# Kernel tuning notes

Measured on AMD Instinct MI355X. Metric: run time of the kernel, lower is better.

The kernel has to match this reference:

```python
import jax, jax.numpy as jnp
import numpy as np

PAD = 0
VALUE_WEIGHT = 5.0
L, D, H, DF, V, T_MAX = 8, 1024, 16, 4096, 4096, 2048
HD = D // H


def _ln(x, w, b, eps=1e-5):
    mu = x.mean(-1, keepdims=True)
    var = ((x - mu) ** 2).mean(-1, keepdims=True)
    return (x - mu) * jax.lax.rsqrt(var + eps) * w + b


def setup_inputs() -> dict:
    key = jax.random.key(0)
    ks = jax.random.split(key, 16)
    s = 0.02
    inp = {
        'input_ids': jax.random.randint(ks[0], (4, 2048), 0, V),
        'targets': jax.random.randint(ks[1], (4, 2048), 0, V),
        'value_mask': jax.random.randint(ks[2], (4, 2048), 0, 2).astype(bool),
        'token_emb': jax.random.normal(ks[3], (V, D), jnp.float32) * s,
        'pos_emb': jax.random.normal(ks[4], (T_MAX, D), jnp.float32) * s,
        'ln1_w': jnp.ones((L, D), jnp.float32), 'ln1_b': jnp.zeros((L, D), jnp.float32),
        'wqkv': jax.random.normal(ks[5], (L, D, 3 * D), jnp.float32) * s,
        'bqkv': jnp.zeros((L, 3 * D), jnp.float32),
        'wproj': jax.random.normal(ks[6], (L, D, D), jnp.float32) * s,
        'bproj': jnp.zeros((L, D), jnp.float32),
        'ln2_w': jnp.ones((L, D), jnp.float32), 'ln2_b': jnp.zeros((L, D), jnp.float32),
        'w1': jax.random.normal(ks[7], (L, D, DF), jnp.float32) * s,
        'b1': jnp.zeros((L, DF), jnp.float32),
        'w2': jax.random.normal(ks[8], (L, DF, D), jnp.float32) * s,
        'b2': jnp.zeros((L, D), jnp.float32),
        'lnf_w': jnp.ones((D,), jnp.float32), 'lnf_b': jnp.zeros((D,), jnp.float32),
    }
    return inp


def reference(input_ids, targets, value_mask, token_emb, pos_emb, ln1_w, ln1_b,
              wqkv, bqkv, wproj, bproj, ln2_w, ln2_b, w1, b1, w2, b2, lnf_w, lnf_b):
    B, T = input_ids.shape
    x = token_emb[input_ids] + pos_emb[:T]  # (B,T,D)
    causal = jnp.triu(jnp.ones((T, T), bool), 1)  # True above diagonal -> masked
    scale = 1.0 / np.sqrt(HD)
    for l in range(L):
        h = _ln(x, ln1_w[l], ln1_b[l])
        qkv = h @ wqkv[l] + bqkv[l]  # (B,T,3D)
        q, k, v = jnp.split(qkv, 3, axis=-1)
        q = q.reshape(B, T, H, HD).transpose(0, 2, 1, 3)  # (B,H,T,HD)
        k = k.reshape(B, T, H, HD).transpose(0, 2, 1, 3)
        v = v.reshape(B, T, H, HD).transpose(0, 2, 1, 3)
        scores = jnp.einsum('bhqd,bhkd->bhqk', q, k) * scale
        scores = jnp.where(causal, -jnp.inf, scores)
        attn = jax.nn.softmax(scores, axis=-1)
        out = jnp.einsum('bhqk,bhkd->bhqd', attn, v)
        out = out.transpose(0, 2, 1, 3).reshape(B, T, D)
        x = x + out @ wproj[l] + bproj[l]
        h2 = _ln(x, ln2_w[l], ln2_b[l])
        x = x + jax.nn.gelu(h2 @ w1[l] + b1[l], approximate=False) @ w2[l] + b2[l]
    x = _ln(x, lnf_w, lnf_b)
    logits = x @ token_emb.T  # tied lm_head, (B,T,V)
    # weighted CE (ignore_index=PAD zeroes the per-token loss; weights sum over all tokens)
    logp = jax.nn.log_softmax(logits, axis=-1)
    nll = -jnp.take_along_axis(logp, targets[..., None], axis=-1)[..., 0]  # (B,T)
    ce = jnp.where(targets == PAD, 0.0, nll)
    weights = 1.0 + (VALUE_WEIGHT - 1.0) * value_mask.astype(jnp.float32)
    loss = (ce * weights).sum() / weights.sum()
    return logits, loss
```

## Files before the change

kernel.cpp:

```cpp
#include <hip/hip_runtime.h>
#include <hip/hip_bf16.h>

typedef unsigned short u16;
typedef short bf16x8 __attribute__((ext_vector_type(8)));
typedef float f32x4 __attribute__((ext_vector_type(4)));

__device__ inline float bflo(unsigned int w) { union { float f; unsigned int i; } c; c.i = w << 16; return c.f; }
__device__ inline float bfhi(unsigned int w) { union { float f; unsigned int i; } c; c.i = w & 0xffff0000u; return c.f; }
__device__ inline u16 f2bf(float f) {
    union { float f; unsigned int i; } c; c.f = f;
    unsigned int r = c.i + 0x7FFFu + ((c.i >> 16) & 1u);
    return (u16)(r >> 16);
}

__device__ inline float wave_sum(float v) {
#pragma unroll
    for (int off = 32; off; off >>= 1) v += __shfl_down(v, off);
    return v;
}

__device__ inline void gload16(const void* g, void* l) {
    __builtin_amdgcn_global_load_lds((const __attribute__((address_space(1))) void*)g,
                                     (__attribute__((address_space(3))) void*)l, 16, 0, 0);
}

__global__ __launch_bounds__(256) void k_cvt(const float* __restrict__ in, u16* __restrict__ out) {
    int i = blockIdx.x * 256 + threadIdx.x;
    float4 v = ((const float4*)in)[i];
    ushort4 o;
    o.x = f2bf(v.x); o.y = f2bf(v.y); o.z = f2bf(v.z); o.w = f2bf(v.w);
    ((ushort4*)out)[i] = o;
}

__global__ __launch_bounds__(256) void k_transpose(const float* __restrict__ in, u16* __restrict__ out, int R, int C) {
    __shared__ float tile[32][33];
    const float* inL = in + (size_t)blockIdx.z * R * C;
    u16* outL = out + (size_t)blockIdx.z * R * C;
    int cb = blockIdx.x * 32, rb = blockIdx.y * 32;
    int tx = threadIdx.x, ty = threadIdx.y;
#pragma unroll
    for (int i = 0; i < 32; i += 8)
        tile[ty + i][tx] = inL[(size_t)(rb + ty + i) * C + cb + tx];
    __syncthreads();
#pragma unroll
    for (int i = 0; i < 32; i += 8)
        outL[(size_t)(cb + ty + i) * R + rb + tx] = f2bf(tile[tx][ty + i]);
}

__global__ __launch_bounds__(256) void k_embed(const int* __restrict__ ids, const float* __restrict__ emb,
                                               const float* __restrict__ pos, float* __restrict__ x) {
    int i = blockIdx.x * 256 + threadIdx.x;
    int m = i >> 8;
    int d4 = i & 255;
    int t = m & 2047;
    int id = ids[m];
    float4 e = ((const float4*)(emb + (size_t)id * 1024))[d4];
    float4 p = ((const float4*)(pos + (size_t)t * 1024))[d4];
    float4 r; r.x = e.x + p.x; r.y = e.y + p.y; r.z = e.z + p.z; r.w = e.w + p.w;
    ((float4*)(x + (size_t)m * 1024))[d4] = r;
}

__global__ __launch_bounds__(256) void k_ln(const float* __restrict__ in, const float* __restrict__ w,
                                            const float* __restrict__ b, u16* __restrict__ out) {
    int row = blockIdx.x, tid = threadIdx.x;
    float4 v = ((const float4*)(in + (size_t)row * 1024))[tid];
    float s = v.x + v.y + v.z + v.w;
    float ss = v.x * v.x + v.y * v.y + v.z * v.z + v.w * v.w;
    s = wave_sum(s); ss = wave_sum(ss);
    __shared__ float rs[4], rss[4];
    int wid = tid >> 6, lane = tid & 63;
    if (lane == 0) { rs[wid] = s; rss[wid] = ss; }
    __syncthreads();
    s = rs[0] + rs[1] + rs[2] + rs[3];
    ss = rss[0] + rss[1] + rss[2] + rss[3];
    float mu = s * (1.0f / 1024.0f);
    float var = ss * (1.0f / 1024.0f) - mu * mu;
    float inv = rsqrtf(var + 1e-5f);
    float4 wv = ((const float4*)w)[tid], bv = ((const float4*)b)[tid];
    ushort4 o;
    o.x = f2bf((v.x - mu) * inv * wv.x + bv.x);
    o.y = f2bf((v.y - mu) * inv * wv.y + bv.y);
    o.z = f2bf((v.z - mu) * inv * wv.z + bv.z);
    o.w = f2bf((v.w - mu) * inv * wv.w + bv.w);
    *(ushort4*)(out + (size_t)row * 1024 + tid * 4) = o;
}

template <bool OUT_BF16, bool GELU, bool RES, bool BIAS>
__global__ __launch_bounds__(256, 2) void k_gemm(const u16* __restrict__ A, const u16* __restrict__ Bt,
                                                 const float* __restrict__ bias, const float* __restrict__ res,
                                                 float* __restrict__ outF, u16* __restrict__ outB,
                                                 int M, int N, int K) {
    __shared__ __align__(16) u16 ldsA[2][128 * 32];
    __shared__ __align__(16) u16 ldsB[2][128 * 32];
    int tid = threadIdx.x;
    int wave = tid >> 6, lane = tid & 63;
    int quad = lane >> 4, l15 = lane & 15;
    int m0 = blockIdx.y * 128, n0 = blockIdx.x * 128;
    int wm = (wave >> 1) * 64, wn = (wave & 1) * 64;

    f32x4 acc[4][4];
#pragma unroll
    for (int i = 0; i < 4; i++)
#pragma unroll
        for (int j = 0; j < 4; j++) acc[i][j] = (f32x4){0.f, 0.f, 0.f, 0.f};

    int r0 = tid >> 2, c0 = (tid & 3) * 8;
    const size_t half = (size_t)64 * K;
    const u16* pa0 = A + (size_t)(m0 + r0) * K + c0;
    const u16* pb0 = Bt + (size_t)(n0 + r0) * K + c0;
    const int woff = (tid & 0xC0) * 8;

#define STAGE(bi, k0)                              \
    {                                              \
        u16* la_ = ldsA[bi] + woff;                \
        u16* lb_ = ldsB[bi] + woff;                \
        gload16(pa0 + (k0), la_);                  \
        gload16(pa0 + half + (k0), la_ + 2048);    \
        gload16(pb0 + (k0), lb_);                  \
        gload16(pb0 + half + (k0), lb_ + 2048);    \
    }

    STAGE(0, 0);
    __syncthreads();

    const int nt = K >> 5;
    int cur = 0;
    for (int t = 0; t < nt; t++) {
        if (t + 1 < nt) STAGE(cur ^ 1, (t + 1) * 32);
        const u16* ca = ldsA[cur];
        const u16* cb = ldsB[cur];
        bf16x8 af[4], bfr[4];
#pragma unroll
        for (int i = 0; i < 4; i++) af[i] = *(const bf16x8*)(ca + (wm + i * 16 + l15) * 32 + quad * 8);
#pragma unroll
        for (int j = 0; j < 4; j++) bfr[j] = *(const bf16x8*)(cb + (wn + j * 16 + l15) * 32 + quad * 8);
#pragma unroll
        for (int i = 0; i < 4; i++)
#pragma unroll
            for (int j = 0; j < 4; j++)
                acc[i][j] = __builtin_amdgcn_mfma_f32_16x16x32_bf16(af[i], bfr[j], acc[i][j], 0, 0, 0);
        __syncthreads();
        cur ^= 1;
    }
#undef STAGE

#pragma unroll
    for (int j = 0; j < 4; j++) {
        int col = n0 + wn + j * 16 + l15;
        float bj = BIAS ? bias[col] : 0.f;
#pragma unroll
        for (int i = 0; i < 4; i++) {
#pragma unroll
            for (int r = 0; r < 4; r++) {
                int row = m0 + wm + i * 16 + quad * 4 + r;
                float v = acc[i][j][r] + bj;
                if (GELU) v = 0.5f * v * (1.0f + erff(v * 0.70710678f));
                if (RES) v += res[(size_t)row * N + col];
                if (OUT_BF16) outB[(size_t)row * N + col] = f2bf(v);
                else outF[(size_t)row * N + col] = v;
            }
        }
    }
}

__global__ __launch_bounds__(256, 2) void k_attn(const u16* __restrict__ qkv, u16* __restrict__ out) {
    const int b = blockIdx.y >> 4, h = blockIdx.y & 15;
    const int qt = gridDim.x - 1 - blockIdx.x;
    const int q0 = qt * 128;
    const int tid = threadIdx.x;
    const int wave = tid >> 6, lane = tid & 63;
    const int quad = lane >> 4, l15 = lane & 15;
    const int wrow = q0 + wave * 32;

    __shared__ __align__(16) u16 Klds[64 * 72];
    __shared__ __align__(16) u16 Vt[64 * 72];
    __shared__ __align__(16) u16 Plds[4][32 * 72];

    const u16* base = qkv + (size_t)b * 2048 * 3072 + h * 64;

    bf16x8 qf[2][2];
#pragma unroll
    for (int i = 0; i < 2; i++)
#pragma unroll
        for (int kc = 0; kc < 2; kc++)
            qf[i][kc] = *(const bf16x8*)(base + (size_t)(wrow + i * 16 + l15) * 3072 + kc * 32 + quad * 8);

    f32x4 o[2][4];
#pragma unroll
    for (int i = 0; i < 2; i++)
#pragma unroll
        for (int jd = 0; jd < 4; jd++) o[i][jd] = (f32x4){0.f, 0.f, 0.f, 0.f};
    float mrow[2][4], lrow[2][4];
#pragma unroll
    for (int i = 0; i < 2; i++)
#pragma unroll
        for (int r = 0; r < 4; r++) { mrow[i][r] = -3e38f; lrow[i][r] = 0.f; }

    const int kk_ = tid >> 2, kc0 = (tid & 3) * 16;
    const int vk = tid & 63, vc = (tid >> 6) * 16;

    const int ktiles = 2 * (qt + 1);
    for (int t = 0; t < ktiles; t++) {
        const int kt = t * 64;
        __syncthreads();
        {
            const u16* kp = base + 1024 + (size_t)(kt + kk_) * 3072 + kc0;
            uint4 a = *(const uint4*)kp;
            uint4 c = *(const uint4*)(kp + 8);
            *(uint4*)(Klds + kk_ * 72 + kc0) = a;
            *(uint4*)(Klds + kk_ * 72 + kc0 + 8) = c;
            const u16* vp = base + 2048 + (size_t)(kt + vk) * 3072 + vc;
            uint4 v0 = *(const uint4*)vp;
            uint4 v1 = *(const uint4*)(vp + 8);
            u16 tmp[16];
            *(uint4*)tmp = v0; *(uint4*)(tmp + 8) = v1;
#pragma unroll
            for (int e = 0; e < 16; e++) Vt[(vc + e) * 72 + vk] = tmp[e];
        }
        __syncthreads();

        if (kt <= wrow + 31) {
            f32x4 s[2][4];
#pragma unroll
            for (int i = 0; i < 2; i++)
#pragma unroll
                for (int j = 0; j < 4; j++) s[i][j] = (f32x4){0.f, 0.f, 0.f, 0.f};
#pragma unroll
            for (int kc = 0; kc < 2; kc++) {
                bf16x8 bf[4];
#pragma unroll
                for (int j = 0; j < 4; j++)
                    bf[j] = *(const bf16x8*)(Klds + (j * 16 + l15) * 72 + kc * 32 + quad * 8);
#pragma unroll
                for (int i = 0; i < 2; i++)
#pragma unroll
                    for (int j = 0; j < 4; j++)
                        s[i][j] = __builtin_amdgcn_mfma_f32_16x16x32_bf16(qf[i][kc], bf[j], s[i][j], 0, 0, 0);
            }
            const bool partial = (kt + 63 > wrow);
#pragma unroll
            for (int i = 0; i < 2; i++)
#pragma unroll
                for (int j = 0; j < 4; j++)
#pragma unroll
                    for (int r = 0; r < 4; r++) {
                        float v = s[i][j][r] * 0.125f;
                        if (partial) {
                            int row = wrow + i * 16 + quad * 4 + r;
                            int col = kt + j * 16 + l15;
                            if (col > row) v = -3e30f;
                        }
                        s[i][j][r] = v;
                    }
            u16* pw = Plds[wave];
#pragma unroll
            for (int i = 0; i < 2; i++)
#pragma unroll
                for (int r = 0; r < 4; r++) {
                    float mx = fmaxf(fmaxf(s[i][0][r], s[i][1][r]), fmaxf(s[i][2][r], s[i][3][r]));
                    mx = fmaxf(mx, __shfl_xor(mx, 1));
                    mx = fmaxf(mx, __shfl_xor(mx, 2));
                    mx = fmaxf(mx, __shfl_xor(mx, 4));
                    mx = fmaxf(mx, __shfl_xor(mx, 8));
                    float mnew = fmaxf(mrow[i][r], mx);
                    float alpha = __expf(mrow[i][r] - mnew);
                    mrow[i][r] = mnew;
                    float psum = 0.f;
#pragma unroll
                    for (int j = 0; j < 4; j++) {
                        float p = __expf(s[i][j][r] - mnew);
                        s[i][j][r] = p;
                        psum += p;
                    }
                    psum += __shfl_xor(psum, 1);
                    psum += __shfl_xor(psum, 2);
                    psum += __shfl_xor(psum, 4);
                    psum += __shfl_xor(psum, 8);
                    lrow[i][r] = lrow[i][r] * alpha + psum;
#pragma unroll
                    for (int jd = 0; jd < 4; jd++) o[i][jd][r] *= alpha;
                }
#pragma unroll
            for (int i = 0; i < 2; i++)
#pragma unroll
                for (int j = 0; j < 4; j++)
#pragma unroll
                    for (int r = 0; r < 4; r++)
                        pw[(i * 16 + quad * 4 + r) * 72 + j * 16 + l15] = f2bf(s[i][j][r]);
#pragma unroll
            for (int kc = 0; kc < 2; kc++) {
                bf16x8 pa[2], vb[4];
#pragma unroll
                for (int i = 0; i < 2; i++)
                    pa[i] = *(const bf16x8*)(pw + (i * 16 + l15) * 72 + kc * 32 + quad * 8);
#pragma unroll
                for (int jd = 0; jd < 4; jd++)
                    vb[jd] = *(const bf16x8*)(Vt + (jd * 16 + l15) * 72 + kc * 32 + quad * 8);
#pragma unroll
                for (int i = 0; i < 2; i++)
#pragma unroll
                    for (int jd = 0; jd < 4; jd++)
                        o[i][jd] = __builtin_amdgcn_mfma_f32_16x16x32_bf16(pa[i], vb[jd], o[i][jd], 0, 0, 0);
            }
        }
    }
#pragma unroll
    for (int i = 0; i < 2; i++)
#pragma unroll
        for (int r = 0; r < 4; r++) {
            float inv = 1.0f / lrow[i][r];
            size_t row = (size_t)(b * 2048 + wrow + i * 16 + quad * 4 + r);
#pragma unroll
            for (int jd = 0; jd < 4; jd++)
                out[row * 1024 + h * 64 + jd * 16 + l15] = f2bf(o[i][jd][r] * inv);
        }
}

__global__ __launch_bounds__(256) void k_ce(const float* __restrict__ logits, const int* __restrict__ targets,
                                            float* __restrict__ ce) {
    int row = blockIdx.x, tid = threadIdx.x;
    const float4* lr = (const float4*)(logits + (size_t)row * 4096);
    float4 v[4];
#pragma unroll
    for (int c = 0; c < 4; c++) v[c] = lr[tid + c * 256];
    float mx = -3e38f;
#pragma unroll
    for (int c = 0; c < 4; c++) mx = fmaxf(mx, fmaxf(fmaxf(v[c].x, v[c].y), fmaxf(v[c].z, v[c].w)));
#pragma unroll
    for (int off = 32; off; off >>= 1) mx = fmaxf(mx, __shfl_xor(mx, off));
    __shared__ float rm[4], rsum[4];
    int wid = tid >> 6, lane = tid & 63;
    if (lane == 0) rm[wid] = mx;
    __syncthreads();
    mx = fmaxf(fmaxf(rm[0], rm[1]), fmaxf(rm[2], rm[3]));
    float se = 0.f;
#pragma unroll
    for (int c = 0; c < 4; c++)
        se += __expf(v[c].x - mx) + __expf(v[c].y - mx) + __expf(v[c].z - mx) + __expf(v[c].w - mx);
#pragma unroll
    for (int off = 32; off; off >>= 1) se += __shfl_xor(se, off);
    if (lane == 0) rsum[wid] = se;
    __syncthreads();
    if (tid == 0) {
        se = rsum[0] + rsum[1] + rsum[2] + rsum[3];
        int tgt = targets[row];
        float nll = -(logits[(size_t)row * 4096 + tgt] - mx - logf(se));
        ce[row] = (tgt == 0) ? 0.f : nll;
    }
}

__global__ __launch_bounds__(256) void k_loss(const float* __restrict__ ce, const int* __restrict__ vmask,
                                              float* __restrict__ out) {
    int tid = threadIdx.x;
    int wid = tid >> 6, lane = tid & 63;
    int bad = 0;
    for (int i = tid; i < 2048; i += 256) {
        unsigned int w = ((const unsigned int*)vmask)[i];
        if (w > 1u) bad = 1;
    }
#pragma unroll
    for (int off = 32; off; off >>= 1) bad |= __shfl_xor(bad, off);
    __shared__ int sb[4];
    if (lane == 0) sb[wid] = bad;
    __syncthreads();
    bad = sb[0] | sb[1] | sb[2] | sb[3];

    float s1 = 0.f, s2 = 0.f;
    if (bad) {
        const unsigned char* mb = (const unsigned char*)vmask;
        for (int i = tid; i < 8192; i += 256) {
            float w = 1.0f + 4.0f * (mb[i] != 0);
            s1 += ce[i] * w; s2 += w;
        }
    } else {
        for (int i = tid; i < 8192; i += 256) {
            float w = 1.0f + 4.0f * (vmask[i] != 0);
            s1 += ce[i] * w; s2 += w;
        }
    }
#pragma unroll
    for (int off = 32; off; off >>= 1) { s1 += __shfl_down(s1, off); s2 += __shfl_down(s2, off); }
    __shared__ float r1[4], r2[4];
    if (lane == 0) { r1[wid] = s1; r2[wid] = s2; }
    __syncthreads();
    if (tid == 0) out[0] = (r1[0] + r1[1] + r1[2] + r1[3]) / (r2[0] + r2[1] + r2[2] + r2[3]);
}

extern "C" void kernel_launch(void* const* d_in, const int* in_sizes, int n_in,
                              void* d_out, int out_size, void* d_ws, size_t ws_size,
                              hipStream_t stream) {
    const int* input_ids = (const int*)d_in[0];
    const int* targets = (const int*)d_in[1];
    const int* vmask = (const int*)d_in[2];
    const float* token_emb = (const float*)d_in[3];
    const float* pos_emb = (const float*)d_in[4];
    const float* ln1_w = (const float*)d_in[5];
    const float* ln1_b = (const float*)d_in[6];
    const float* wqkv = (const float*)d_in[7];
    const float* bqkv = (const float*)d_in[8];
    const float* wproj = (const float*)d_in[9];
    const float* bproj = (const float*)d_in[10];
    const float* ln2_w = (const float*)d_in[11];
    const float* ln2_b = (const float*)d_in[12];
    const float* w1 = (const float*)d_in[13];
    const float* b1 = (const float*)d_in[14];
    const float* w2 = (const float*)d_in[15];
    const float* b2 = (const float*)d_in[16];
    const float* lnf_w = (const float*)d_in[17];
    const float* lnf_b = (const float*)d_in[18];

    char* p = (char*)d_ws;
    u16* embb = (u16*)p;   p += (size_t)4096 * 1024 * 2;
    u16* wqkvt = (u16*)p;  p += (size_t)8 * 3072 * 1024 * 2;
    u16* wprojt = (u16*)p; p += (size_t)8 * 1024 * 1024 * 2;
    u16* w1t = (u16*)p;    p += (size_t)8 * 4096 * 1024 * 2;
    u16* w2t = (u16*)p;    p += (size_t)8 * 1024 * 4096 * 2;
    float* xw = (float*)p; p += (size_t)8192 * 1024 * 4;
    u16* hb = (u16*)p;     p += (size_t)8192 * 1024 * 2;
    u16* qkvb = (u16*)p;   p += (size_t)8192 * 3072 * 2;
    u16* attnb = (u16*)p;  p += (size_t)8192 * 1024 * 2;
    u16* ffb = (u16*)p;    p += (size_t)8192 * 4096 * 2;
    float* cerow = (float*)p; p += 8192 * 4;

    float* logits = (float*)d_out;

    k_cvt<<<4096, 256, 0, stream>>>(token_emb, embb);
    dim3 tb(32, 8);
    k_transpose<<<dim3(96, 32, 8), tb, 0, stream>>>(wqkv, wqkvt, 1024, 3072);
    k_transpose<<<dim3(32, 32, 8), tb, 0, stream>>>(wproj, wprojt, 1024, 1024);
    k_transpose<<<dim3(128, 32, 8), tb, 0, stream>>>(w1, w1t, 1024, 4096);
    k_transpose<<<dim3(32, 128, 8), tb, 0, stream>>>(w2, w2t, 4096, 1024);

    k_embed<<<8192, 256, 0, stream>>>(input_ids, token_emb, pos_emb, xw);

    for (int l = 0; l < 8; l++) {
        k_ln<<<8192, 256, 0, stream>>>(xw, ln1_w + l * 1024, ln1_b + l * 1024, hb);
        k_gemm<true, false, false, true><<<dim3(24, 64), 256, 0, stream>>>(
            hb, wqkvt + (size_t)l * 3072 * 1024, bqkv + l * 3072, nullptr, nullptr, qkvb, 8192, 3072, 1024);
        k_attn<<<dim3(16, 64), 256, 0, stream>>>(qkvb, attnb);
        k_gemm<false, false, true, true><<<dim3(8, 64), 256, 0, stream>>>(
            attnb, wprojt + (size_t)l * 1024 * 1024, bproj + l * 1024, xw, xw, nullptr, 8192, 1024, 1024);
        k_ln<<<8192, 256, 0, stream>>>(xw, ln2_w + l * 1024, ln2_b + l * 1024, hb);
        k_gemm<true, true, false, true><<<dim3(32, 64), 256, 0, stream>>>(
            hb, w1t + (size_t)l * 4096 * 1024, b1 + l * 4096, nullptr, nullptr, ffb, 8192, 4096, 1024);
        k_gemm<false, false, true, true><<<dim3(8, 64), 256, 0, stream>>>(
            ffb, w2t + (size_t)l * 1024 * 4096, b2 + l * 1024, xw, xw, nullptr, 8192, 1024, 4096);
    }

    k_ln<<<8192, 256, 0, stream>>>(xw, lnf_w, lnf_b, hb);
    k_gemm<false, false, false, false><<<dim3(32, 64), 256, 0, stream>>>(
        hb, embb, nullptr, nullptr, logits, nullptr, 8192, 4096, 1024);

    k_ce<<<8192, 256, 0, stream>>>(logits, targets, cerow);
    k_loss<<<1, 256, 0, stream>>>(cerow, vmask, logits + (size_t)8192 * 4096);
}
```

Measured before the change: 5.170 ms.

## Add 256x256 pipelined GEMM for wide projections and balance causal attention tiles

Adds a 512-thread GEMM kernel with 256x256 output tiles. It uses double-buffered LDS filled by direct global-to-LDS loads, an XOR-swizzled layout, split-phase prefetch, and priority hints around the MFMA bursts. The kernel is used for the QKV, FFN-up and LM-head GEMMs to raise data reuse per tile and overlap loads with compute. Attention blocks now each handle a pair of query tiles (qt and 15-qt), halving the grid so every block does similar work under the causal mask. The costs are high register pressure from the 8x4 accumulators (launch bounds ask for 2 blocks of 512 threads) and fewer blocks per launch, which hurts the tail on small grids.

```diff
diff --git a/kernel.cpp b/kernel.cpp
--- a/kernel.cpp
+++ b/kernel.cpp
@@ -5,8 +5,6 @@
 typedef short bf16x8 __attribute__((ext_vector_type(8)));
 typedef float f32x4 __attribute__((ext_vector_type(4)));
 
-__device__ inline float bflo(unsigned int w) { union { float f; unsigned int i; } c; c.i = w << 16; return c.f; }
-__device__ inline float bfhi(unsigned int w) { union { float f; unsigned int i; } c; c.i = w & 0xffff0000u; return c.f; }
 __device__ inline u16 f2bf(float f) {
     union { float f; unsigned int i; } c; c.f = f;
     unsigned int r = c.i + 0x7FFFu + ((c.i >> 16) & 1u);
@@ -163,14 +161,149 @@
     }
 }
 
+template <bool OUT_BF16, bool GELU, bool BIAS>
+__global__ __launch_bounds__(512, 2) void k_gemm256(const u16* __restrict__ A, const u16* __restrict__ Bt,
+                                                    const float* __restrict__ bias,
+                                                    float* __restrict__ outF, u16* __restrict__ outB,
+                                                    int M, int N, int K) {
+    __shared__ __align__(16) u16 As[2][256 * 64];
+    __shared__ __align__(16) u16 Bs[2][256 * 64];
+    const int tid = threadIdx.x;
+    const int lane = tid & 63;
+    const int quad = lane >> 4, l15 = lane & 15;
+    const int m0 = blockIdx.y * 256, n0 = blockIdx.x * 256;
+    const int wm = ((tid >> 6) >> 2) * 128;
+    const int wn = ((tid >> 6) & 3) * 64;
+    const int NT = K >> 6;
+
+    f32x4 acc[8][4];
+#pragma unroll
+    for (int i = 0; i < 8; i++)
+#pragma unroll
+        for (int j = 0; j < 4; j++) acc[i][j] = (f32x4){0.f, 0.f, 0.f, 0.f};
+
+    const int rS = tid >> 3;
+    const int cSwz = ((tid & 7) * 16) ^ ((rS & 7) << 4);
+    const u16* gA = A + (size_t)(m0 + rS) * K + (cSwz >> 1);
+    const u16* gB = Bt + (size_t)(n0 + rS) * K + (cSwz >> 1);
+
+    auto issue_half = [&](int t, int j) {
+        if (t >= NT) return;
+        const int bf = t & 1;
+        if (j <= 1) {
+            const u16* src = gA + (size_t)(j * 128) * K + (size_t)t * 64;
+            u16* dst = &As[bf][j * 8192 + tid * 8];
+            gload16(src, dst);
+            gload16(src + (size_t)64 * K, dst + 4096);
+        } else {
+            const int h = j - 2;
+            const u16* src = gB + (size_t)(h * 128) * K + (size_t)t * 64;
+            u16* dst = &Bs[bf][h * 8192 + tid * 8];
+            gload16(src, dst);
+            gload16(src + (size_t)64 * K, dst + 4096);
+        }
+    };
+    auto ldA = [&](int bf, int mi, int ks) {
+        int r = wm + mi * 16 + l15;
+        int cb = (ks * 64 + quad * 16) ^ ((r & 7) << 4);
+        return *(const bf16x8*)((const char*)&As[bf][0] + (size_t)r * 128 + cb);
+    };
+    auto ldB = [&](int bf, int nj, int ks) {
+        int r = wn + nj * 16 + l15;
+        int cb = (ks * 64 + quad * 16) ^ ((r & 7) << 4);
+        return *(const bf16x8*)((const char*)&Bs[bf][0] + (size_t)r * 128 + cb);
+    };
+
+    issue_half(0, 0); issue_half(0, 1); issue_half(0, 2); issue_half(0, 3);
+    issue_half(1, 0);
+    asm volatile("s_waitcnt vmcnt(2)" ::: "memory");
+    __builtin_amdgcn_s_barrier();
+
+    for (int t = 0; t < NT; t++) {
+        const int bf = t & 1;
+        bf16x8 a0[4], a1[4], b0[4], b1[4];
+#pragma unroll
+        for (int mi = 0; mi < 4; mi++) a0[mi] = ldA(bf, mi, 0);
+#pragma unroll
+        for (int nj = 0; nj < 4; nj++) b0[nj] = ldB(bf, nj, 0);
+        issue_half(t + 1, 1);
+        __builtin_amdgcn_s_barrier();
+        __builtin_amdgcn_s_setprio(1);
+#pragma unroll
+        for (int mi = 0; mi < 4; mi++)
+#pragma unroll
+            for (int nj = 0; nj < 4; nj++)
+                acc[mi][nj] = __builtin_amdgcn_mfma_f32_16x16x32_bf16(a0[mi], b0[nj], acc[mi][nj], 0, 0, 0);
+        __builtin_amdgcn_s_setprio(0);
+        __builtin_amdgcn_s_barrier();
+#pragma unroll
+        for (int mi = 0; mi < 4; mi++) a1[mi] = ldA(bf, mi, 1);
+#pragma unroll
+        for (int nj = 0; nj < 4; nj++) b1[nj] = ldB(bf, nj, 1);
+        issue_half(t + 1, 2);
+        __builtin_amdgcn_s_barrier();
+        __builtin_amdgcn_s_setprio(1);
+#pragma unroll
+        for (int mi = 0; mi < 4; mi++)
+#pragma unroll
+            for (int nj = 0; nj < 4; nj++)
+                acc[mi][nj] = __builtin_amdgcn_mfma_f32_16x16x32_bf16(a1[mi], b1[nj], acc[mi][nj], 0, 0, 0);
+        __builtin_amdgcn_s_setprio(0);
+        __builtin_amdgcn_s_barrier();
+#pragma unroll
+        for (int mi = 0; mi < 4; mi++) a0[mi] = ldA(bf, mi + 4, 0);
+#pragma unroll
+        for (int mi = 0; mi < 4; mi++) a1[mi] = ldA(bf, mi + 4, 1);
+        issue_half(t + 1, 3);
+        __builtin_amdgcn_s_barrier();
+        __builtin_amdgcn_s_setprio(1);
+#pragma unroll
+        for (int mi = 0; mi < 4; mi++)
+#pragma unroll
+            for (int nj = 0; nj < 4; nj++)
+                acc[mi + 4][nj] = __builtin_amdgcn_mfma_f32_16x16x32_bf16(a0[mi], b0[nj], acc[mi + 4][nj], 0, 0, 0);
+        __builtin_amdgcn_s_setprio(0);
+        __builtin_amdgcn_s_barrier();
+        issue_half(t + 2, 0);
+        __builtin_amdgcn_s_barrier();
+        __builtin_amdgcn_s_setprio(1);
+#pragma unroll
+        for (int mi = 0; mi < 4; mi++)
+#pragma unroll
+            for (int nj = 0; nj < 4; nj++)
+                acc[mi + 4][nj] = __builtin_amdgcn_mfma_f32_16x16x32_bf16(a1[mi], b1[nj], acc[mi + 4][nj], 0, 0, 0);
+        __builtin_amdgcn_s_setprio(0);
+        if (t + 2 < NT) {
+            asm volatile("s_waitcnt vmcnt(2)" ::: "memory");
+        } else {
+            asm volatile("s_waitcnt vmcnt(0)" ::: "memory");
+        }
+        __builtin_amdgcn_s_barrier();
+    }
+
+#pragma unroll
+    for (int nj = 0; nj < 4; nj++) {
+        int col = n0 + wn + nj * 16 + l15;
+        float bj = BIAS ? bias[col] : 0.f;
+#pragma unroll
+        for (int mi = 0; mi < 8; mi++) {
+#pragma unroll
+            for (int r = 0; r < 4; r++) {
+                int row = m0 + wm + mi * 16 + quad * 4 + r;
+                float v = acc[mi][nj][r] + bj;
+                if (GELU) v = 0.5f * v * (1.0f + erff(v * 0.70710678f));
+                if (OUT_BF16) outB[(size_t)row * N + col] = f2bf(v);
+                else outF[(size_t)row * N + col] = v;
+            }
+        }
+    }
+}
+
 __global__ __launch_bounds__(256, 2) void k_attn(const u16* __restrict__ qkv, u16* __restrict__ out) {
     const int b = blockIdx.y >> 4, h = blockIdx.y & 15;
-    const int qt = gridDim.x - 1 - blockIdx.x;
-    const int q0 = qt * 128;
     const int tid = threadIdx.x;
     const int wave = tid >> 6, lane = tid & 63;
     const int quad = lane >> 4, l15 = lane & 15;
-    const int wrow = q0 + wave * 32;
 
     __shared__ __align__(16) u16 Klds[64 * 72];
     __shared__ __align__(16) u16 Vt[64 * 72];
@@ -178,142 +311,148 @@
 
     const u16* base = qkv + (size_t)b * 2048 * 3072 + h * 64;
 
-    bf16x8 qf[2][2];
-#pragma unroll
-    for (int i = 0; i < 2; i++)
-#pragma unroll
-        for (int kc = 0; kc < 2; kc++)
-            qf[i][kc] = *(const bf16x8*)(base + (size_t)(wrow + i * 16 + l15) * 3072 + kc * 32 + quad * 8);
-
-    f32x4 o[2][4];
-#pragma unroll
-    for (int i = 0; i < 2; i++)
-#pragma unroll
-        for (int jd = 0; jd < 4; jd++) o[i][jd] = (f32x4){0.f, 0.f, 0.f, 0.f};
-    float mrow[2][4], lrow[2][4];
-#pragma unroll
-    for (int i = 0; i < 2; i++)
-#pragma unroll
-        for (int r = 0; r < 4; r++) { mrow[i][r] = -3e38f; lrow[i][r] = 0.f; }
-
     const int kk_ = tid >> 2, kc0 = (tid & 3) * 16;
     const int vk = tid & 63, vc = (tid >> 6) * 16;
 
-    const int ktiles = 2 * (qt + 1);
-    for (int t = 0; t < ktiles; t++) {
-        const int kt = t * 64;
-        __syncthreads();
-        {
-            const u16* kp = base + 1024 + (size_t)(kt + kk_) * 3072 + kc0;
-            uint4 a = *(const uint4*)kp;
-            uint4 c = *(const uint4*)(kp + 8);
-            *(uint4*)(Klds + kk_ * 72 + kc0) = a;
-            *(uint4*)(Klds + kk_ * 72 + kc0 + 8) = c;
-            const u16* vp = base + 2048 + (size_t)(kt + vk) * 3072 + vc;
-            uint4 v0 = *(const uint4*)vp;
-            uint4 v1 = *(const uint4*)(vp + 8);
-            u16 tmp[16];
-            *(uint4*)tmp = v0; *(uint4*)(tmp + 8) = v1;
-#pragma unroll
-            for (int e = 0; e < 16; e++) Vt[(vc + e) * 72 + vk] = tmp[e];
-        }
-        __syncthreads();
-
-        if (kt <= wrow + 31) {
-            f32x4 s[2][4];
-#pragma unroll
-            for (int i = 0; i < 2; i++)
-#pragma unroll
-                for (int j = 0; j < 4; j++) s[i][j] = (f32x4){0.f, 0.f, 0.f, 0.f};
-#pragma unroll
-            for (int kc = 0; kc < 2; kc++) {
-                bf16x8 bf[4];
-#pragma unroll
-                for (int j = 0; j < 4; j++)
-                    bf[j] = *(const bf16x8*)(Klds + (j * 16 + l15) * 72 + kc * 32 + quad * 8);
+    for (int pass = 0; pass < 2; pass++) {
+        const int qt = pass ? blockIdx.x : 15 - blockIdx.x;
+        const int q0 = qt * 128;
+        const int wrow = q0 + wave * 32;
+
+        bf16x8 qf[2][2];
+#pragma unroll
+        for (int i = 0; i < 2; i++)
+#pragma unroll
+            for (int kc = 0; kc < 2; kc++)
+                qf[i][kc] = *(const bf16x8*)(base + (size_t)(wrow + i * 16 + l15) * 3072 + kc * 32 + quad * 8);
+
+        f32x4 o[2][4];
+#pragma unroll
+        for (int i = 0; i < 2; i++)
+#pragma unroll
+            for (int jd = 0; jd < 4; jd++) o[i][jd] = (f32x4){0.f, 0.f, 0.f, 0.f};
+        float mrow[2][4], lrow[2][4];
+#pragma unroll
+        for (int i = 0; i < 2; i++)
+#pragma unroll
+            for (int r = 0; r < 4; r++) { mrow[i][r] = -3e38f; lrow[i][r] = 0.f; }
+
+        const int ktiles = 2 * (qt + 1);
+        for (int t = 0; t < ktiles; t++) {
+            const int kt = t * 64;
+            __syncthreads();
+            {
+                const u16* kp = base + 1024 + (size_t)(kt + kk_) * 3072 + kc0;
+                uint4 a = *(const uint4*)kp;
+                uint4 c = *(const uint4*)(kp + 8);
+                *(uint4*)(Klds + kk_ * 72 + kc0) = a;
+                *(uint4*)(Klds + kk_ * 72 + kc0 + 8) = c;
+                const u16* vp = base + 2048 + (size_t)(kt + vk) * 3072 + vc;
+                uint4 v0 = *(const uint4*)vp;
+                uint4 v1 = *(const uint4*)(vp + 8);
+                u16 tmp[16];
+                *(uint4*)tmp = v0; *(uint4*)(tmp + 8) = v1;
+#pragma unroll
+                for (int e = 0; e < 16; e++) Vt[(vc + e) * 72 + vk] = tmp[e];
+            }
+            __syncthreads();
+
+            if (kt <= wrow + 31) {
+                f32x4 s[2][4];
 #pragma unroll
                 for (int i = 0; i < 2; i++)
 #pragma unroll
+                    for (int j = 0; j < 4; j++) s[i][j] = (f32x4){0.f, 0.f, 0.f, 0.f};
+#pragma unroll
+                for (int kc = 0; kc < 2; kc++) {
+                    bf16x8 bf[4];
+#pragma unroll
                     for (int j = 0; j < 4; j++)
-                        s[i][j] = __builtin_amdgcn_mfma_f32_16x16x32_bf16(qf[i][kc], bf[j], s[i][j], 0, 0, 0);
+                        bf[j] = *(const bf16x8*)(Klds + (j * 16 + l15) * 72 + kc * 32 + quad * 8);
+#pragma unroll
+                    for (int i = 0; i < 2; i++)
+#pragma unroll
+                        for (int j = 0; j < 4; j++)
+                            s[i][j] = __builtin_amdgcn_mfma_f32_16x16x32_bf16(qf[i][kc], bf[j], s[i][j], 0, 0, 0);
+                }
+                const bool partial = (kt + 63 > wrow);
+#pragma unroll
+                for (int i = 0; i < 2; i++)
+#pragma unroll
+                    for (int j = 0; j < 4; j++)
+#pragma unroll
+                        for (int r = 0; r < 4; r++) {
+                            float v = s[i][j][r] * 0.125f;
+                            if (partial) {
+                                int row = wrow + i * 16 + quad * 4 + r;
+                                int col = kt + j * 16 + l15;
+                                if (col > row) v = -3e30f;
+                            }
+                            s[i][j][r] = v;
+                        }
+                u16* pw = Plds[wave];
+#pragma unroll
+                for (int i = 0; i < 2; i++)
+#pragma unroll
+                    for (int r = 0; r < 4; r++) {
+                        float mx = fmaxf(fmaxf(s[i][0][r], s[i][1][r]), fmaxf(s[i][2][r], s[i][3][r]));
+                        mx = fmaxf(mx, __shfl_xor(mx, 1));
+                        mx = fmaxf(mx, __shfl_xor(mx, 2));
+                        mx = fmaxf(mx, __shfl_xor(mx, 4));
+                        mx = fmaxf(mx, __shfl_xor(mx, 8));
+                        float mnew = fmaxf(mrow[i][r], mx);
+                        float alpha = __expf(mrow[i][r] - mnew);
+                        mrow[i][r] = mnew;
+                        float psum = 0.f;
+#pragma unroll
+                        for (int j = 0; j < 4; j++) {
+                            float p = __expf(s[i][j][r] - mnew);
+                            s[i][j][r] = p;
+                            psum += p;
+                        }
+                        psum += __shfl_xor(psum, 1);
+                        psum += __shfl_xor(psum, 2);
+                        psum += __shfl_xor(psum, 4);
+                        psum += __shfl_xor(psum, 8);
+                        lrow[i][r] = lrow[i][r] * alpha + psum;
+#pragma unroll
+                        for (int jd = 0; jd < 4; jd++) o[i][jd][r] *= alpha;
+                    }
+#pragma unroll
+                for (int i = 0; i < 2; i++)
+#pragma unroll
+                    for (int j = 0; j < 4; j++)
+#pragma unroll
+                        for (int r = 0; r < 4; r++)
+                            pw[(i * 16 + quad * 4 + r) * 72 + j * 16 + l15] = f2bf(s[i][j][r]);
+#pragma unroll
+                for (int kc = 0; kc < 2; kc++) {
+                    bf16x8 pa[2], vb[4];
+#pragma unroll
+                    for (int i = 0; i < 2; i++)
+                        pa[i] = *(const bf16x8*)(pw + (i * 16 + l15) * 72 + kc * 32 + quad * 8);
+#pragma unroll
+                    for (int jd = 0; jd < 4; jd++)
+                        vb[jd] = *(const bf16x8*)(Vt + (jd * 16 + l15) * 72 + kc * 32 + quad * 8);
+#pragma unroll
+                    for (int i = 0; i < 2; i++)
+#pragma unroll
+                        for (int jd = 0; jd < 4; jd++)
+                            o[i][jd] = __builtin_amdgcn_mfma_f32_16x16x32_bf16(pa[i], vb[jd], o[i][jd], 0, 0, 0);
+                }
             }
-            const bool partial = (kt + 63 > wrow);
-#pragma unroll
-            for (int i = 0; i < 2; i++)
-#pragma unroll
-                for (int j = 0; j < 4; j++)
-#pragma unroll
-                    for (int r = 0; r < 4; r++) {
-                        float v = s[i][j][r] * 0.125f;
-                        if (partial) {
-                            int row = wrow + i * 16 + quad * 4 + r;
-                            int col = kt + j * 16 + l15;
-                            if (col > row) v = -3e30f;
-                        }
-                        s[i][j][r] = v;
-                    }
-            u16* pw = Plds[wave];
-#pragma unroll
-            for (int i = 0; i < 2; i++)
-#pragma unroll
-                for (int r = 0; r < 4; r++) {
-                    float mx = fmaxf(fmaxf(s[i][0][r], s[i][1][r]), fmaxf(s[i][2][r], s[i][3][r]));
-                    mx = fmaxf(mx, __shfl_xor(mx, 1));
-                    mx = fmaxf(mx, __shfl_xor(mx, 2));
-                    mx = fmaxf(mx, __shfl_xor(mx, 4));
-                    mx = fmaxf(mx, __shfl_xor(mx, 8));
-                    float mnew = fmaxf(mrow[i][r], mx);
-                    float alpha = __expf(mrow[i][r] - mnew);
-                    mrow[i][r] = mnew;
-                    float psum = 0.f;
-#pragma unroll
-                    for (int j = 0; j < 4; j++) {
-                        float p = __expf(s[i][j][r] - mnew);
-                        s[i][j][r] = p;
-                        psum += p;
-                    }
-                    psum += __shfl_xor(psum, 1);
-                    psum += __shfl_xor(psum, 2);
-                    psum += __shfl_xor(psum, 4);
-                    psum += __shfl_xor(psum, 8);
-                    lrow[i][r] = lrow[i][r] * alpha + psum;
-#pragma unroll
-                    for (int jd = 0; jd < 4; jd++) o[i][jd][r] *= alpha;
-                }
-#pragma unroll
-            for (int i = 0; i < 2; i++)
-#pragma unroll
-                for (int j = 0; j < 4; j++)
-#pragma unroll
-                    for (int r = 0; r < 4; r++)
-                        pw[(i * 16 + quad * 4 + r) * 72 + j * 16 + l15] = f2bf(s[i][j][r]);
-#pragma unroll
-            for (int kc = 0; kc < 2; kc++) {
-                bf16x8 pa[2], vb[4];
-#pragma unroll
-                for (int i = 0; i < 2; i++)
-                    pa[i] = *(const bf16x8*)(pw + (i * 16 + l15) * 72 + kc * 32 + quad * 8);
+        }
+#pragma unroll
+        for (int i = 0; i < 2; i++)
+#pragma unroll
+            for (int r = 0; r < 4; r++) {
+                float inv = 1.0f / lrow[i][r];
+                size_t row = (size_t)(b * 2048 + wrow + i * 16 + quad * 4 + r);
 #pragma unroll
                 for (int jd = 0; jd < 4; jd++)
-                    vb[jd] = *(const bf16x8*)(Vt + (jd * 16 + l15) * 72 + kc * 32 + quad * 8);
-#pragma unroll
-                for (int i = 0; i < 2; i++)
-#pragma unroll
-                    for (int jd = 0; jd < 4; jd++)
-                        o[i][jd] = __builtin_amdgcn_mfma_f32_16x16x32_bf16(pa[i], vb[jd], o[i][jd], 0, 0, 0);
+                    out[row * 1024 + h * 64 + jd * 16 + l15] = f2bf(o[i][jd][r] * inv);
             }
-        }
-    }
-#pragma unroll
-    for (int i = 0; i < 2; i++)
-#pragma unroll
-        for (int r = 0; r < 4; r++) {
-            float inv = 1.0f / lrow[i][r];
-            size_t row = (size_t)(b * 2048 + wrow + i * 16 + quad * 4 + r);
-#pragma unroll
-            for (int jd = 0; jd < 4; jd++)
-                out[row * 1024 + h * 64 + jd * 16 + l15] = f2bf(o[i][jd][r] * inv);
-        }
+    }
 }
 
 __global__ __launch_bounds__(256) void k_ce(const float* __restrict__ logits, const int* __restrict__ targets,
@@ -435,21 +574,21 @@
 
     for (int l = 0; l < 8; l++) {
         k_ln<<<8192, 256, 0, stream>>>(xw, ln1_w + l * 1024, ln1_b + l * 1024, hb);
-        k_gemm<true, false, false, true><<<dim3(24, 64), 256, 0, stream>>>(
-            hb, wqkvt + (size_t)l * 3072 * 1024, bqkv + l * 3072, nullptr, nullptr, qkvb, 8192, 3072, 1024);
-        k_attn<<<dim3(16, 64), 256, 0, stream>>>(qkvb, attnb);
+        k_gemm256<true, false, true><<<dim3(12, 32), 512, 0, stream>>>(
+            hb, wqkvt + (size_t)l * 3072 * 1024, bqkv + l * 3072, nullptr, qkvb, 8192, 3072, 1024);
+        k_attn<<<dim3(8, 64), 256, 0, stream>>>(qkvb, attnb);
         k_gemm<false, false, true, true><<<dim3(8, 64), 256, 0, stream>>>(
             attnb, wprojt + (size_t)l * 1024 * 1024, bproj + l * 1024, xw, xw, nullptr, 8192, 1024, 1024);
         k_ln<<<8192, 256, 0, stream>>>(xw, ln2_w + l * 1024, ln2_b + l * 1024, hb);
-        k_gemm<true, true, false, true><<<dim3(32, 64), 256, 0, stream>>>(
-            hb, w1t + (size_t)l * 4096 * 1024, b1 + l * 4096, nullptr, nullptr, ffb, 8192, 4096, 1024);
+        k_gemm256<true, true, true><<<dim3(16, 32), 512, 0, stream>>>(
+            hb, w1t + (size_t)l * 4096 * 1024, b1 + l * 4096, nullptr, ffb, 8192, 4096, 1024);
         k_gemm<false, false, true, true><<<dim3(8, 64), 256, 0, stream>>>(
             ffb, w2t + (size_t)l * 1024 * 4096, b2 + l * 1024, xw, xw, nullptr, 8192, 1024, 4096);
     }
 
     k_ln<<<8192, 256, 0, stream>>>(xw, lnf_w, lnf_b, hb);
-    k_gemm<false, false, false, false><<<dim3(32, 64), 256, 0, stream>>>(
-        hb, embb, nullptr, nullptr, logits, nullptr, 8192, 4096, 1024);
+    k_gemm256<false, false, false><<<dim3(16, 32), 512, 0, stream>>>(
+        hb, embb, nullptr, logits, nullptr, 8192, 4096, 1024);
 
     k_ce<<<8192, 256, 0, stream>>>(logits, targets, cerow);
     k_loss<<<1, 256, 0, stream>>>(cerow, vmask, logits + (size_t)8192 * 4096);
```

Result: faster. 4.983 ms (-3.6%).
